# Kernel tuning notes

Hardware: AMD Instinct MI355X
Metric: run time of the kernel (lower is better)

## Reference

```python
import jax, jax.numpy as jnp
import numpy as np

BINS = 32
MAX_DIST = 128
EMB = 1024
DQ = 64
DV = 64
H = 16
B = 8
L = 1024


def _t5_bucket_table():
    # matches: clamp(n,max=m) + (log(clamp(n,min=m)-m+1)*(bins-1-m)/log(max_distance-m+1)).long()
    n = np.arange(MAX_DIST + 1)
    m = BINS // 2
    idx = np.minimum(n, m) + (
        np.log(np.maximum(n, m) - m + 1) * (BINS - 1 - m) / np.log(MAX_DIST - m + 1)
    ).astype(np.int64)
    return jnp.asarray(idx)


def setup_inputs() -> dict:
    key = jax.random.key(0)
    ks = jax.random.split(key, 8)
    s = 0.02
    return {
        "x": jax.random.normal(ks[0], (B, L, EMB), dtype=jnp.float32),
        "qk_w": jax.random.normal(ks[1], (2 * DQ * H, EMB), dtype=jnp.float32) * s,
        "qk_b": jnp.zeros((2 * DQ * H,), dtype=jnp.float32),
        "v_w": jax.random.normal(ks[2], (DV * H, EMB), dtype=jnp.float32) * s,
        "v_b": jnp.zeros((DV * H,), dtype=jnp.float32),
        "out_w": jax.random.normal(ks[3], (EMB, DV * H), dtype=jnp.float32) * s,
        "out_b": jnp.zeros((EMB,), dtype=jnp.float32),
        "bias": jax.random.normal(ks[4], (BINS, H), dtype=jnp.float32) * s,  # causal -> bins rows
    }


def reference(x, qk_w, qk_b, v_w, v_b, out_w, out_b, bias):
    # projections
    qk = (x @ qk_w.T + qk_b).reshape(B, L, H, 2 * DQ).transpose(0, 2, 1, 3)  # [B,H,L,2DQ]
    q, k = qk[..., :DQ], qk[..., DQ:]
    v = (x @ v_w.T + v_b).reshape(B, L, H, DV).transpose(0, 2, 1, 3)  # [B,H,L,DV]

    # T5 relative-position bias (causal): gather per (i-j) distance bucket
    idx_tab = _t5_bucket_table()
    shifts = jnp.arange(L)[:, None] - jnp.arange(L)[None, :]  # [L,L], i - j
    bins_idx = idx_tab[jnp.clip(jnp.abs(shifts), 0, MAX_DIST)]  # [L,L]
    bmat = bias[bins_idx].transpose(2, 0, 1)  # [H,L,L]
    bmat = jnp.where(shifts < 0, -jnp.inf, bmat)  # causal mask (j > i)

    scale = 1.0 / np.sqrt(DQ).astype(np.float32)
    scores = jnp.einsum("bhid,bhjd->bhij", q, k) * scale + bmat  # [B,H,L,L]
    attn = jax.nn.softmax(scores, axis=-1)
    out = jnp.einsum("bhij,bhjd->bhid", attn, v)  # [B,H,L,DV]
    out = out.transpose(0, 2, 1, 3).reshape(B, L, H * DV)
    return out @ out_w.T + out_b
```

## Files before the change

kernel.cpp:

```cpp
#include <hip/hip_runtime.h>
#include <cmath>


typedef _Float16 f16x8 __attribute__((ext_vector_type(8)));
typedef _Float16 f16x4 __attribute__((ext_vector_type(4)));
typedef float    f32x4 __attribute__((ext_vector_type(4)));

#define NEG_INF (-__builtin_inff())
#define LOG2E 1.4426950408889634f

#if __has_builtin(__builtin_amdgcn_exp2f)
#define EXP2(x) __builtin_amdgcn_exp2f(x)
#else
#define EXP2(x) exp2f(x)
#endif

__device__ __forceinline__ void gl_lds16(const void* g, void* l) {
  __builtin_amdgcn_global_load_lds(
      (__attribute__((address_space(1))) void*)g,
      (__attribute__((address_space(3))) void*)l,
      16, 0, 0);
}

__device__ __forceinline__ f32x4 mfma32(f16x8 a, f16x8 b, f32x4 c) {
  return __builtin_amdgcn_mfma_f32_16x16x32_f16(a, b, c, 0, 0, 0);
}
__device__ __forceinline__ f32x4 mfma16(f16x4 a, f16x4 b, f32x4 c) {
  return __builtin_amdgcn_mfma_f32_16x16x16f16(a, b, c, 0, 0, 0);
}

typedef __attribute__((address_space(3))) _Float16* lds_f16p;

#define DSR(d, a, o) \
  asm volatile("ds_read_b128 %0, %1 offset:" o : "=v"(d) : "v"(a))

#define GEMM_VM4 asm volatile("s_waitcnt vmcnt(4)" ::: "memory")
#define GEMM_VM3 asm volatile("s_waitcnt vmcnt(3)" ::: "memory")
#define GEMM_VM0 asm volatile("s_waitcnt vmcnt(0)" ::: "memory")
#define GEMM_BAR __builtin_amdgcn_s_barrier()

#define GEMM_COMPUTE(aB, bB)                             \
  do {                                                   \
    f16x8 af0, af1, af2, af3, bf0, bf1, bf2, bf3;        \
    DSR(af0, aB, "0");                                   \
    DSR(bf0, bB, "0");                                   \
    DSR(af1, aB, "1024");                                \
    DSR(bf1, bB, "1024");                                \
    DSR(af2, aB, "2048");                                \
    DSR(bf2, bB, "2048");                                \
    DSR(af3, aB, "3072");                                \
    DSR(bf3, bB, "3072");                                \
    asm volatile("s_waitcnt lgkmcnt(4)" ::: "memory");   \
    __builtin_amdgcn_sched_barrier(0);                   \
    __builtin_amdgcn_s_setprio(1);                       \
    acc[0][0] = mfma32(af0, bf0, acc[0][0]);             \
    acc[0][1] = mfma32(af0, bf1, acc[0][1]);             \
    acc[1][0] = mfma32(af1, bf0, acc[1][0]);             \
    acc[1][1] = mfma32(af1, bf1, acc[1][1]);             \
    asm volatile("s_waitcnt lgkmcnt(0)" ::: "memory");   \
    __builtin_amdgcn_sched_barrier(0);                   \
    acc[0][2] = mfma32(af0, bf2, acc[0][2]);             \
    acc[0][3] = mfma32(af0, bf3, acc[0][3]);             \
    acc[1][2] = mfma32(af1, bf2, acc[1][2]);             \
    acc[1][3] = mfma32(af1, bf3, acc[1][3]);             \
    acc[2][0] = mfma32(af2, bf0, acc[2][0]);             \
    acc[2][1] = mfma32(af2, bf1, acc[2][1]);             \
    acc[2][2] = mfma32(af2, bf2, acc[2][2]);             \
    acc[2][3] = mfma32(af2, bf3, acc[2][3]);             \
    acc[3][0] = mfma32(af3, bf0, acc[3][0]);             \
    acc[3][1] = mfma32(af3, bf1, acc[3][1]);             \
    acc[3][2] = mfma32(af3, bf2, acc[3][2]);             \
    acc[3][3] = mfma32(af3, bf3, acc[3][3]);             \
    __builtin_amdgcn_s_setprio(0);                       \
  } while (0)

__global__ void cvt4_kernel(const float* __restrict__ x,
                            const float* __restrict__ w1,
                            const float* __restrict__ w2,
                            const float* __restrict__ w3,
                            _Float16* __restrict__ ox, _Float16* __restrict__ o1,
                            _Float16* __restrict__ o2, _Float16* __restrict__ o3) {
  const int bid = blockIdx.x;
  const float* src;
  _Float16* dst;
  int idx;
  if (bid < 8192) {
    src = x; dst = ox; idx = bid * 256 + threadIdx.x;
  } else if (bid < 10240) {
    src = w1; dst = o1; idx = (bid - 8192) * 256 + threadIdx.x;
  } else if (bid < 11264) {
    src = w2; dst = o2; idx = (bid - 10240) * 256 + threadIdx.x;
  } else {
    src = w3; dst = o3; idx = (bid - 11264) * 256 + threadIdx.x;
  }
  float4 v = reinterpret_cast<const float4*>(src)[idx];
  f16x4 o;
  o[0] = (_Float16)v.x; o[1] = (_Float16)v.y;
  o[2] = (_Float16)v.z; o[3] = (_Float16)v.w;
  reinterpret_cast<f16x4*>(dst)[idx] = o;
}

#define GEMM_STAGE256(buf, kk)                                \
  do {                                                        \
    gl_lds16(pA0 + (kk), &lds[(buf)*8192 + wof]);             \
    gl_lds16(pA1 + (kk), &lds[(buf)*8192 + 4096 + wof]);      \
    gl_lds16(pB0 + (kk), &lds[24576 + (buf)*4096 + wof]);     \
  } while (0)

__global__ __launch_bounds__(512, 4) void gemm256_kernel(
    const _Float16* __restrict__ A, const _Float16* __restrict__ Bm,
    const float* __restrict__ bias_q, const float* __restrict__ bias_v,
    _Float16* __restrict__ qkbuf, _Float16* __restrict__ vtbuf) {
  const int K = 1024;
  __shared__ __align__(16) _Float16 lds[36864];
  const int t = threadIdx.x;
  const int w = t >> 6;
  const int lane = t & 63;
  const int lq = lane & 15, lg = lane >> 4;
  const int wr = w >> 1, wc = w & 1;
  const int m0 = blockIdx.y * 256, n0 = blockIdx.x * 128;

  const int stc = ((t & 3) ^ ((t >> 3) & 3)) * 8;
  const _Float16* pA0 = A + (size_t)(m0 + (t >> 2)) * K + stc;
  const _Float16* pA1 = pA0 + (size_t)128 * K;
  const _Float16* pB0 = Bm + (size_t)(n0 + (t >> 2)) * K + stc;
  const int wof = w * 512;

  const int xsw = (lq >> 1) & 3;
  const uint32_t base = (uint32_t)(uintptr_t)(lds_f16p)&lds[0];
  const uint32_t aB0 =
      base + (uint32_t)((wr * 64 + lq) * 64 + ((lg ^ xsw) << 4));
  const uint32_t aB1 = aB0 + 16384;
  const uint32_t aB2 = aB0 + 32768;
  const uint32_t bB0 =
      base + 49152 + (uint32_t)((wc * 64 + lq) * 64 + ((lg ^ xsw) << 4));
  const uint32_t bB1 = bB0 + 8192;
  const uint32_t bB2 = bB0 + 16384;

  f32x4 acc[4][4];
#pragma unroll
  for (int mi = 0; mi < 4; ++mi)
#pragma unroll
    for (int ni = 0; ni < 4; ++ni) acc[mi][ni] = (f32x4){0.f, 0.f, 0.f, 0.f};

  GEMM_STAGE256(0, 0);
  GEMM_STAGE256(1, 32);
  for (int kt = 0; kt < 960; kt += 96) {
    GEMM_VM3;
    GEMM_BAR;
    GEMM_STAGE256(2, kt + 64);
    GEMM_COMPUTE(aB0, bB0);
    GEMM_VM3;
    GEMM_BAR;
    GEMM_STAGE256(0, kt + 96);
    GEMM_COMPUTE(aB1, bB1);
    GEMM_VM3;
    GEMM_BAR;
    GEMM_STAGE256(1, kt + 128);
    GEMM_COMPUTE(aB2, bB2);
  }
  GEMM_VM3;
  GEMM_BAR;
  GEMM_COMPUTE(aB0, bB0);
  GEMM_VM0;
  GEMM_BAR;
  GEMM_COMPUTE(aB1, bB1);

  GEMM_BAR;
  _Float16* T = &lds[0];
  const bool isqk = (n0 < 2048);
  const int bb = m0 >> 10, ii0 = m0 & 1023;
  if (isqk) {
#pragma unroll
    for (int mi = 0; mi < 4; ++mi)
#pragma unroll
      for (int ni = 0; ni < 4; ++ni) {
        const int col = wc * 64 + ni * 16 + lq;
        const float bq = bias_q[n0 + col];
#pragma unroll
        for (int r = 0; r < 4; ++r) {
          const int row = wr * 64 + mi * 16 + lg * 4 + r;
          T[row * 136 + col] = (_Float16)(acc[mi][ni][r] + bq);
        }
      }
    __syncthreads();
    const int hh = n0 >> 7;
    _Float16* gb = qkbuf + ((size_t)((bb * 16 + hh) * 1024 + ii0)) * 128;
    const int row = t >> 1, half = t & 1;
    const int so = row * 136 + half * 64;
    const int go = row * 128 + half * 64;
#pragma unroll
    for (int j = 0; j < 8; ++j)
      *(f16x8*)(gb + go + j * 8) = *(const f16x8*)&T[so + j * 8];
  } else {
    const int nn0 = n0 - 2048;
#pragma unroll
    for (int mi = 0; mi < 4; ++mi)
#pragma unroll
      for (int ni = 0; ni < 4; ++ni) {
        const int col = wc * 64 + ni * 16 + lq;
        const float bv = bias_v[nn0 + col];
        const int row0 = wr * 64 + mi * 16 + lg * 4;
        f16x4 p;
#pragma unroll
        for (int r = 0; r < 4; ++r) p[r] = (_Float16)(acc[mi][ni][r] + bv);
        *(f16x4*)&T[col * 264 + row0] = p;
      }
    __syncthreads();
    const int c = t >> 2, qd = t & 3;
    const int nn = nn0 + c;
    const int hh = nn >> 6, dv = nn & 63;
    _Float16* gb = vtbuf + ((size_t)((bb * 16 + hh) * 64 + dv)) * 1024 +
                   ii0 + qd * 64;
    const int so = c * 264 + qd * 64;
#pragma unroll
    for (int j = 0; j < 8; ++j)
      *(f16x8*)(gb + j * 8) = *(const f16x8*)&T[so + j * 8];
  }
}

#define GEMM_STAGE128(buf, kk)                                     \
  do {                                                             \
    gl_lds16(pA0 + (kk), &lds[(buf)*4096 + wof]);                  \
    gl_lds16(pA1 + (kk), &lds[(buf)*4096 + 2048 + wof]);           \
    gl_lds16(pB0 + (kk), &lds[12288 + (buf)*4096 + wof]);          \
    gl_lds16(pB1 + (kk), &lds[12288 + (buf)*4096 + 2048 + wof]);   \
  } while (0)

__global__ __launch_bounds__(256, 3) void gemm128_kernel(
    const _Float16* __restrict__ A, const _Float16* __restrict__ Bm,
    const float* __restrict__ bias_o, float* __restrict__ outf) {
  const int K = 1024, N = 1024;
  __shared__ __align__(16) _Float16 lds[6 * 4096];
  const int t = threadIdx.x;
  const int w = t >> 6;
  const int lane = t & 63;
  const int lq = lane & 15, lg = lane >> 4;
  const int wr = w >> 1, wc = w & 1;
  const int m0 = blockIdx.y * 128, n0 = blockIdx.x * 128;

  const int stc = ((t & 3) ^ ((t >> 3) & 3)) * 8;
  const _Float16* pA0 = A + (size_t)(m0 + (t >> 2)) * K + stc;
  const _Float16* pA1 = pA0 + (size_t)64 * K;
  const _Float16* pB0 = Bm + (size_t)(n0 + (t >> 2)) * K + stc;
  const _Float16* pB1 = pB0 + (size_t)64 * K;
  const int wof = w * 512;

  const int xsw = (lq >> 1) & 3;
  const uint32_t base = (uint32_t)(uintptr_t)(lds_f16p)&lds[0];
  const uint32_t aB0 =
      base + (uint32_t)((wr * 64 + lq) * 64 + ((lg ^ xsw) << 4));
  const uint32_t aB1 = aB0 + 8192;
  const uint32_t aB2 = aB0 + 16384;
  const uint32_t bB0 =
      base + 24576 + (uint32_t)((wc * 64 + lq) * 64 + ((lg ^ xsw) << 4));
  const uint32_t bB1 = bB0 + 8192;
  const uint32_t bB2 = bB0 + 16384;

  f32x4 acc[4][4];
#pragma unroll
  for (int mi = 0; mi < 4; ++mi)
#pragma unroll
    for (int ni = 0; ni < 4; ++ni) acc[mi][ni] = (f32x4){0.f, 0.f, 0.f, 0.f};

  GEMM_STAGE128(0, 0);
  GEMM_STAGE128(1, 32);
  for (int kt = 0; kt < 960; kt += 96) {
    GEMM_VM4;
    GEMM_BAR;
    GEMM_STAGE128(2, kt + 64);
    GEMM_COMPUTE(aB0, bB0);
    GEMM_VM4;
    GEMM_BAR;
    GEMM_STAGE128(0, kt + 96);
    GEMM_COMPUTE(aB1, bB1);
    GEMM_VM4;
    GEMM_BAR;
    GEMM_STAGE128(1, kt + 128);
    GEMM_COMPUTE(aB2, bB2);
  }
  GEMM_VM4;
  GEMM_BAR;
  GEMM_COMPUTE(aB0, bB0);
  GEMM_VM0;
  GEMM_BAR;
  GEMM_COMPUTE(aB1, bB1);

#pragma unroll
  for (int mi = 0; mi < 4; ++mi)
#pragma unroll
    for (int ni = 0; ni < 4; ++ni)
#pragma unroll
      for (int r = 0; r < 4; ++r) {
        const int mg = m0 + wr * 64 + mi * 16 + lg * 4 + r;
        const int ng = n0 + wc * 64 + ni * 16 + lq;
        outf[(size_t)mg * N + ng] = acc[mi][ni][r] + bias_o[ng];
      }
}

__device__ __forceinline__ void stage_kv(const _Float16* __restrict__ kb,
                                         const _Float16* __restrict__ vtb,
                                         int j0, _Float16* kl, _Float16* vl,
                                         int t) {
  const int r0 = t >> 3, c0 = t & 7;
  const int r1 = r0 + 32;
  const int kc0 = c0 ^ (r0 & 7), kc1 = c0 ^ (r1 & 7);
  gl_lds16(kb + (size_t)(j0 + r0) * 128 + kc0 * 8, kl + t * 8);
  gl_lds16(kb + (size_t)(j0 + r1) * 128 + kc1 * 8, kl + (t + 256) * 8);
  gl_lds16(vtb + (size_t)r0 * 1024 + j0 + kc0 * 8, vl + t * 8);
  gl_lds16(vtb + (size_t)r1 * 1024 + j0 + kc1 * 8, vl + (t + 256) * 8);
}

__device__ __forceinline__ void softmax16(f32x4 (&st)[4], f16x4 (&ph)[4],
                                          int qi, int j0, bool far,
                                          const float* __restrict__ tab,
                                          float t128, int lg4, float& m_run,
                                          float& l_part, f32x4 (&oacc)[4]) {
  float xs[16];
  float lmax = NEG_INF;
  if (far) {
#pragma unroll
    for (int js = 0; js < 4; ++js)
#pragma unroll
      for (int r = 0; r < 4; ++r) {
        const float xv = fmaf(st[js][r], 0.125f * LOG2E, t128);
        xs[js * 4 + r] = xv;
        lmax = fmaxf(lmax, xv);
      }
  } else {
#pragma unroll
    for (int js = 0; js < 4; ++js)
#pragma unroll
      for (int r = 0; r < 4; ++r) {
        const int jj = j0 + js * 16 + lg4 + r;
        const int dd = qi - jj;
        const int idx = dd < 0 ? 0 : (dd > 128 ? 128 : dd);
        const float xv =
            (dd < 0) ? NEG_INF : fmaf(st[js][r], 0.125f * LOG2E, tab[idx]);
        xs[js * 4 + r] = xv;
        lmax = fmaxf(lmax, xv);
      }
  }
  if (__any(lmax > m_run + 8.0f)) {
    float tmax = fmaxf(lmax, __shfl_xor(lmax, 16));
    tmax = fmaxf(tmax, __shfl_xor(tmax, 32));
    const float m_new = fmaxf(m_run, tmax);
    const float sf = EXP2(m_run - m_new);
    m_run = m_new;
    l_part *= sf;
    f32x4 sfv;
#pragma unroll
    for (int r = 0; r < 4; ++r) sfv[r] = __shfl(sf, lg4 + r);
#pragma unroll
    for (int db = 0; db < 4; ++db) oacc[db] *= sfv;
  }
  float ls = 0.f;
#pragma unroll
  for (int js = 0; js < 4; ++js)
#pragma unroll
    for (int r = 0; r < 4; ++r) {
      const float p = EXP2(xs[js * 4 + r] - m_run);
      ls += p;
      ph[js][r] = (_Float16)p;
    }
  l_part += ls;
}

__global__ __launch_bounds__(256, 4) void attn_kernel(
    const _Float16* __restrict__ qk,
    const _Float16* __restrict__ vt,
    const float* __restrict__ bias,
    _Float16* __restrict__ ao) {
  __shared__ __align__(16) _Float16 kls[2][64 * 64];
  __shared__ __align__(16) _Float16 vls[2][64 * 64];
  __shared__ float tab[132];
  const int t = threadIdx.x;
  const int bid = blockIdx.x;
  const int bh = (bid & 7) * 16 + (bid >> 6);
  const int b4 = (bid >> 3) & 7;
  const int h = bh & 15, b = bh >> 4;
  if (t < 129) {
    const int bucket =
        (t <= 16) ? t : 16 + (int)(log((double)(t - 15)) * 15.0 / log(113.0));
    tab[t] = bias[bucket * 16 + h] * LOG2E;
  }

  const int w = t >> 6, lane = t & 63;
  const int lq = lane & 15, lg = lane >> 4;
  const int lg4 = lg * 4, lg8 = lg * 8;
  const int tA = b4, tB = 15 - b4;
  const int q0A = tA * 64 + w * 16, q0B = tB * 64 + w * 16;
  const int qA = q0A + lq, qB = q0B + lq;
  const _Float16* qkb = qk + (size_t)bh * 1024 * 128;
  const _Float16* kb = qkb + 64;
  const _Float16* vtb = vt + (size_t)bh * 64 * 1024;

  const f16x8 qfA0 = *(const f16x8*)&qkb[qA * 128 + lg8];
  const f16x8 qfA1 = *(const f16x8*)&qkb[qA * 128 + 32 + lg8];
  const f16x8 qfB0 = *(const f16x8*)&qkb[qB * 128 + lg8];
  const f16x8 qfB1 = *(const f16x8*)&qkb[qB * 128 + 32 + lg8];

  f32x4 oA[4], oB[4];
#pragma unroll
  for (int db = 0; db < 4; ++db) {
    oA[db] = (f32x4){0.f, 0.f, 0.f, 0.f};
    oB[db] = (f32x4){0.f, 0.f, 0.f, 0.f};
  }
  float mA = NEG_INF, lAp = 0.f, mB = NEG_INF, lBp = 0.f;

  stage_kv(kb, vtb, 0, kls[0], vls[0], t);
  __syncthreads();
  const float t128 = tab[128];
  const int krsw = lq & 7;
  const int vsw = (lq & 7) << 1;
  int cur = 0;

  for (int jt = 0; jt <= tB; ++jt) {
    const int j0 = jt * 64;
    if (jt < tB) stage_kv(kb, vtb, j0 + 64, kls[cur ^ 1], vls[cur ^ 1], t);
    const bool aact = (jt <= tA);
    const _Float16* kbf = kls[cur];
    const _Float16* vbf = vls[cur];

    f32x4 stA[4], stB[4];
#pragma unroll
    for (int js = 0; js < 4; ++js) {
      const int rowb = (js * 16 + lq) * 64;
      const f16x8 kf0 = *(const f16x8*)&kbf[rowb + ((lg ^ krsw) << 3)];
      const f16x8 kf1 = *(const f16x8*)&kbf[rowb + (((lg + 4) ^ krsw) << 3)];
      if (aact) {
        stA[js] = mfma32(kf0, qfA0, (f32x4){0.f, 0.f, 0.f, 0.f});
        stA[js] = mfma32(kf1, qfA1, stA[js]);
      }
      stB[js] = mfma32(kf0, qfB0, (f32x4){0.f, 0.f, 0.f, 0.f});
      stB[js] = mfma32(kf1, qfB1, stB[js]);
    }

    f16x4 phA[4], phB[4];
    if (aact)
      softmax16(stA, phA, qA, j0, q0A - j0 >= 192, tab, t128, lg4, mA, lAp,
                oA);
    softmax16(stB, phB, qB, j0, q0B - j0 >= 192, tab, t128, lg4, mB, lBp, oB);

#pragma unroll
    for (int js = 0; js < 4; ++js)
#pragma unroll
      for (int db = 0; db < 4; ++db) {
        const f16x4 vf = *(const f16x4*)&vbf[(db * 16 + lq) * 64 +
                                             ((((js << 2) + lg) ^ vsw) << 2)];
        if (aact) oA[db] = mfma16(phA[js], vf, oA[db]);
        oB[db] = mfma16(phB[js], vf, oB[db]);
      }

    __syncthreads();
    cur ^= 1;
  }

  _Float16* aob = ao + ((size_t)b * 1024) * 1024 + h * 64;
  {
    float lt = lAp + __shfl_xor(lAp, 16);
    lt += __shfl_xor(lt, 32);
    f32x4 linv;
#pragma unroll
    for (int r = 0; r < 4; ++r) linv[r] = 1.0f / __shfl(lt, lg4 + r);
#pragma unroll
    for (int db = 0; db < 4; ++db)
#pragma unroll
      for (int r = 0; r < 4; ++r)
        aob[(size_t)(q0A + lg4 + r) * 1024 + db * 16 + lq] =
            (_Float16)(oA[db][r] * linv[r]);
  }
  {
    float lt = lBp + __shfl_xor(lBp, 16);
    lt += __shfl_xor(lt, 32);
    f32x4 linv;
#pragma unroll
    for (int r = 0; r < 4; ++r) linv[r] = 1.0f / __shfl(lt, lg4 + r);
#pragma unroll
    for (int db = 0; db < 4; ++db)
#pragma unroll
      for (int r = 0; r < 4; ++r)
        aob[(size_t)(q0B + lg4 + r) * 1024 + db * 16 + lq] =
            (_Float16)(oB[db][r] * linv[r]);
  }
}

extern "C" void kernel_launch(void* const* d_in, const int* in_sizes, int n_in,
                              void* d_out, int out_size, void* d_ws,
                              size_t ws_size, hipStream_t stream) {
  const float* x = (const float*)d_in[0];
  const float* qk_w = (const float*)d_in[1];
  const float* qk_b = (const float*)d_in[2];
  const float* v_w = (const float*)d_in[3];
  const float* v_b = (const float*)d_in[4];
  const float* out_w = (const float*)d_in[5];
  const float* out_b = (const float*)d_in[6];
  const float* bias = (const float*)d_in[7];
  float* out = (float*)d_out;

  _Float16* xb = (_Float16*)d_ws;
  _Float16* wb = xb + (size_t)8388608;
  _Float16* owb = wb + (size_t)3145728;
  _Float16* qkbuf = owb + (size_t)1048576;
  _Float16* vtbuf = qkbuf + (size_t)16777216;
  _Float16* ao = vtbuf + (size_t)8388608;

  cvt4_kernel<<<12288, 256, 0, stream>>>(x, qk_w, v_w, out_w, xb, wb,
                                         wb + 2097152, owb);

  gemm256_kernel<<<dim3(24, 32), 512, 0, stream>>>(xb, wb, qk_b, v_b, qkbuf,
                                                   vtbuf);

  attn_kernel<<<1024, 256, 0, stream>>>(qkbuf, vtbuf, bias, ao);

  gemm128_kernel<<<dim3(8, 64), 256, 0, stream>>>(ao, owb, out_b, out);
}
```

Measured before the change: 162.7 us.

## Use 4-wave 256x128 QKV GEMM tile with larger per-wave 64x128 subtiles

The QKV projection GEMM keeps its 256x128 block tile but moves from 8 waves (512 threads), each computing 64x64, to 4 waves (256 threads), each computing 64x128 with a 4x8 MFMA accumulator grid. Each wave now reuses its A fragments across twice as many B fragments, which cuts LDS read traffic per MFMA, and staging issues six global-to-LDS loads per thread instead of three. The cost is much higher register pressure (128 accumulator VGPRs plus 12 fragment registers), occupancy held to 2 blocks per CU, and fewer waves available to hide latency. The epilogue writes are reworked to match the new thread count.

```diff
diff --git a/kernel.cpp b/kernel.cpp
--- a/kernel.cpp
+++ b/kernel.cpp
@@ -34,10 +34,192 @@
 #define DSR(d, a, o) \
   asm volatile("ds_read_b128 %0, %1 offset:" o : "=v"(d) : "v"(a))
 
+#define GEMM_VM6 asm volatile("s_waitcnt vmcnt(6)" ::: "memory")
 #define GEMM_VM4 asm volatile("s_waitcnt vmcnt(4)" ::: "memory")
-#define GEMM_VM3 asm volatile("s_waitcnt vmcnt(3)" ::: "memory")
 #define GEMM_VM0 asm volatile("s_waitcnt vmcnt(0)" ::: "memory")
 #define GEMM_BAR __builtin_amdgcn_s_barrier()
+
+__global__ void cvt4_kernel(const float* __restrict__ x,
+                            const float* __restrict__ w1,
+                            const float* __restrict__ w2,
+                            const float* __restrict__ w3,
+                            _Float16* __restrict__ ox, _Float16* __restrict__ o1,
+                            _Float16* __restrict__ o2, _Float16* __restrict__ o3) {
+  const int bid = blockIdx.x;
+  const float* src;
+  _Float16* dst;
+  int idx;
+  if (bid < 8192) {
+    src = x; dst = ox; idx = bid * 256 + threadIdx.x;
+  } else if (bid < 10240) {
+    src = w1; dst = o1; idx = (bid - 8192) * 256 + threadIdx.x;
+  } else if (bid < 11264) {
+    src = w2; dst = o2; idx = (bid - 10240) * 256 + threadIdx.x;
+  } else {
+    src = w3; dst = o3; idx = (bid - 11264) * 256 + threadIdx.x;
+  }
+  float4 v = reinterpret_cast<const float4*>(src)[idx];
+  f16x4 o;
+  o[0] = (_Float16)v.x; o[1] = (_Float16)v.y;
+  o[2] = (_Float16)v.z; o[3] = (_Float16)v.w;
+  reinterpret_cast<f16x4*>(dst)[idx] = o;
+}
+
+#define GEMM_STAGEW(buf, kk)                                        \
+  do {                                                              \
+    gl_lds16(pA0 + (kk), &lds[(buf)*8192 + wof]);                   \
+    gl_lds16(pA1 + (kk), &lds[(buf)*8192 + 2048 + wof]);            \
+    gl_lds16(pA2 + (kk), &lds[(buf)*8192 + 4096 + wof]);            \
+    gl_lds16(pA3 + (kk), &lds[(buf)*8192 + 6144 + wof]);            \
+    gl_lds16(pB0 + (kk), &lds[24576 + (buf)*4096 + wof]);           \
+    gl_lds16(pB1 + (kk), &lds[24576 + (buf)*4096 + 2048 + wof]);    \
+  } while (0)
+
+#define GEMM_COMPUTEW(aB, bB)                                  \
+  do {                                                         \
+    f16x8 af[4], bf[8];                                        \
+    DSR(af[0], aB, "0");                                       \
+    DSR(af[1], aB, "1024");                                    \
+    DSR(af[2], aB, "2048");                                    \
+    DSR(af[3], aB, "3072");                                    \
+    DSR(bf[0], bB, "0");                                       \
+    DSR(bf[1], bB, "1024");                                    \
+    DSR(bf[2], bB, "2048");                                    \
+    DSR(bf[3], bB, "3072");                                    \
+    DSR(bf[4], bB, "4096");                                    \
+    DSR(bf[5], bB, "5120");                                    \
+    DSR(bf[6], bB, "6144");                                    \
+    DSR(bf[7], bB, "7168");                                    \
+    asm volatile("s_waitcnt lgkmcnt(6)" ::: "memory");         \
+    __builtin_amdgcn_sched_barrier(0);                         \
+    __builtin_amdgcn_s_setprio(1);                             \
+    _Pragma("unroll") for (int mi = 0; mi < 4; ++mi)           \
+      _Pragma("unroll") for (int ni = 0; ni < 2; ++ni)         \
+        acc[mi][ni] = mfma32(af[mi], bf[ni], acc[mi][ni]);     \
+    asm volatile("s_waitcnt lgkmcnt(0)" ::: "memory");         \
+    __builtin_amdgcn_sched_barrier(0);                         \
+    _Pragma("unroll") for (int mi = 0; mi < 4; ++mi)           \
+      _Pragma("unroll") for (int ni = 2; ni < 8; ++ni)         \
+        acc[mi][ni] = mfma32(af[mi], bf[ni], acc[mi][ni]);     \
+    __builtin_amdgcn_s_setprio(0);                             \
+  } while (0)
+
+__global__ __launch_bounds__(256, 2) void gemmw_kernel(
+    const _Float16* __restrict__ A, const _Float16* __restrict__ Bm,
+    const float* __restrict__ bias_q, const float* __restrict__ bias_v,
+    _Float16* __restrict__ qkbuf, _Float16* __restrict__ vtbuf) {
+  const int K = 1024;
+  __shared__ __align__(16) _Float16 lds[36864];
+  const int t = threadIdx.x;
+  const int w = t >> 6;
+  const int lane = t & 63;
+  const int lq = lane & 15, lg = lane >> 4;
+  const int m0 = blockIdx.y * 256, n0 = blockIdx.x * 128;
+
+  const int stc = ((t & 3) ^ ((t >> 3) & 3)) * 8;
+  const _Float16* pA0 = A + (size_t)(m0 + (t >> 2)) * K + stc;
+  const _Float16* pA1 = pA0 + (size_t)64 * K;
+  const _Float16* pA2 = pA0 + (size_t)128 * K;
+  const _Float16* pA3 = pA0 + (size_t)192 * K;
+  const _Float16* pB0 = Bm + (size_t)(n0 + (t >> 2)) * K + stc;
+  const _Float16* pB1 = pB0 + (size_t)64 * K;
+  const int wof = w * 512;
+
+  const int xsw = (lq >> 1) & 3;
+  const uint32_t base = (uint32_t)(uintptr_t)(lds_f16p)&lds[0];
+  const uint32_t aB0 =
+      base + (uint32_t)((w * 64 + lq) * 64 + ((lg ^ xsw) << 4));
+  const uint32_t aB1 = aB0 + 16384;
+  const uint32_t aB2 = aB0 + 32768;
+  const uint32_t bB0 =
+      base + 49152 + (uint32_t)(lq * 64 + ((lg ^ xsw) << 4));
+  const uint32_t bB1 = bB0 + 8192;
+  const uint32_t bB2 = bB0 + 16384;
+
+  f32x4 acc[4][8];
+#pragma unroll
+  for (int mi = 0; mi < 4; ++mi)
+#pragma unroll
+    for (int ni = 0; ni < 8; ++ni) acc[mi][ni] = (f32x4){0.f, 0.f, 0.f, 0.f};
+
+  GEMM_STAGEW(0, 0);
+  GEMM_STAGEW(1, 32);
+  for (int kt = 0; kt < 960; kt += 96) {
+    GEMM_VM6;
+    GEMM_BAR;
+    GEMM_STAGEW(2, kt + 64);
+    GEMM_COMPUTEW(aB0, bB0);
+    GEMM_VM6;
+    GEMM_BAR;
+    GEMM_STAGEW(0, kt + 96);
+    GEMM_COMPUTEW(aB1, bB1);
+    GEMM_VM6;
+    GEMM_BAR;
+    GEMM_STAGEW(1, kt + 128);
+    GEMM_COMPUTEW(aB2, bB2);
+  }
+  GEMM_VM6;
+  GEMM_BAR;
+  GEMM_COMPUTEW(aB0, bB0);
+  GEMM_VM0;
+  GEMM_BAR;
+  GEMM_COMPUTEW(aB1, bB1);
+
+  GEMM_BAR;
+  _Float16* T = &lds[0];
+  const bool isqk = (n0 < 2048);
+  const int bb = m0 >> 10, ii0 = m0 & 1023;
+  if (isqk) {
+#pragma unroll
+    for (int mi = 0; mi < 4; ++mi)
+#pragma unroll
+      for (int ni = 0; ni < 8; ++ni) {
+        const int col = ni * 16 + lq;
+        const float bq = bias_q[n0 + col];
+#pragma unroll
+        for (int r = 0; r < 4; ++r) {
+          const int row = w * 64 + mi * 16 + lg * 4 + r;
+          T[row * 136 + col] = (_Float16)(acc[mi][ni][r] + bq);
+        }
+      }
+    __syncthreads();
+    const int hh = n0 >> 7;
+    _Float16* gb = qkbuf + ((size_t)((bb * 16 + hh) * 1024 + ii0)) * 128;
+#pragma unroll
+    for (int h2 = 0; h2 < 2; ++h2) {
+      const int row = h2 * 128 + (t >> 1);
+      const int so = row * 136 + (t & 1) * 64;
+      const int go = row * 128 + (t & 1) * 64;
+#pragma unroll
+      for (int j = 0; j < 8; ++j)
+        *(f16x8*)(gb + go + j * 8) = *(const f16x8*)&T[so + j * 8];
+    }
+  } else {
+    const int nn0 = n0 - 2048;
+#pragma unroll
+    for (int mi = 0; mi < 4; ++mi)
+#pragma unroll
+      for (int ni = 0; ni < 8; ++ni) {
+        const int col = ni * 16 + lq;
+        const float bv = bias_v[nn0 + col];
+        const int row0 = w * 64 + mi * 16 + lg * 4;
+        f16x4 p;
+#pragma unroll
+        for (int r = 0; r < 4; ++r) p[r] = (_Float16)(acc[mi][ni][r] + bv);
+        *(f16x4*)&T[col * 264 + row0] = p;
+      }
+    __syncthreads();
+    const int c = t >> 1, half = t & 1;
+    const int nn = nn0 + c;
+    const int hh = nn >> 6, dv = nn & 63;
+    _Float16* gb = vtbuf + ((size_t)((bb * 16 + hh) * 64 + dv)) * 1024 +
+                   ii0 + half * 128;
+    const int so = c * 264 + half * 128;
+#pragma unroll
+    for (int j = 0; j < 16; ++j)
+      *(f16x8*)(gb + j * 8) = *(const f16x8*)&T[so + j * 8];
+  }
+}
 
 #define GEMM_COMPUTE(aB, bB)                             \
   do {                                                   \
@@ -74,151 +256,6 @@
     __builtin_amdgcn_s_setprio(0);                       \
   } while (0)
 
-__global__ void cvt4_kernel(const float* __restrict__ x,
-                            const float* __restrict__ w1,
-                            const float* __restrict__ w2,
-                            const float* __restrict__ w3,
-                            _Float16* __restrict__ ox, _Float16* __restrict__ o1,
-                            _Float16* __restrict__ o2, _Float16* __restrict__ o3) {
-  const int bid = blockIdx.x;
-  const float* src;
-  _Float16* dst;
-  int idx;
-  if (bid < 8192) {
-    src = x; dst = ox; idx = bid * 256 + threadIdx.x;
-  } else if (bid < 10240) {
-    src = w1; dst = o1; idx = (bid - 8192) * 256 + threadIdx.x;
-  } else if (bid < 11264) {
-    src = w2; dst = o2; idx = (bid - 10240) * 256 + threadIdx.x;
-  } else {
-    src = w3; dst = o3; idx = (bid - 11264) * 256 + threadIdx.x;
-  }
-  float4 v = reinterpret_cast<const float4*>(src)[idx];
-  f16x4 o;
-  o[0] = (_Float16)v.x; o[1] = (_Float16)v.y;
-  o[2] = (_Float16)v.z; o[3] = (_Float16)v.w;
-  reinterpret_cast<f16x4*>(dst)[idx] = o;
-}
-
-#define GEMM_STAGE256(buf, kk)                                \
-  do {                                                        \
-    gl_lds16(pA0 + (kk), &lds[(buf)*8192 + wof]);             \
-    gl_lds16(pA1 + (kk), &lds[(buf)*8192 + 4096 + wof]);      \
-    gl_lds16(pB0 + (kk), &lds[24576 + (buf)*4096 + wof]);     \
-  } while (0)
-
-__global__ __launch_bounds__(512, 4) void gemm256_kernel(
-    const _Float16* __restrict__ A, const _Float16* __restrict__ Bm,
-    const float* __restrict__ bias_q, const float* __restrict__ bias_v,
-    _Float16* __restrict__ qkbuf, _Float16* __restrict__ vtbuf) {
-  const int K = 1024;
-  __shared__ __align__(16) _Float16 lds[36864];
-  const int t = threadIdx.x;
-  const int w = t >> 6;
-  const int lane = t & 63;
-  const int lq = lane & 15, lg = lane >> 4;
-  const int wr = w >> 1, wc = w & 1;
-  const int m0 = blockIdx.y * 256, n0 = blockIdx.x * 128;
-
-  const int stc = ((t & 3) ^ ((t >> 3) & 3)) * 8;
-  const _Float16* pA0 = A + (size_t)(m0 + (t >> 2)) * K + stc;
-  const _Float16* pA1 = pA0 + (size_t)128 * K;
-  const _Float16* pB0 = Bm + (size_t)(n0 + (t >> 2)) * K + stc;
-  const int wof = w * 512;
-
-  const int xsw = (lq >> 1) & 3;
-  const uint32_t base = (uint32_t)(uintptr_t)(lds_f16p)&lds[0];
-  const uint32_t aB0 =
-      base + (uint32_t)((wr * 64 + lq) * 64 + ((lg ^ xsw) << 4));
-  const uint32_t aB1 = aB0 + 16384;
-  const uint32_t aB2 = aB0 + 32768;
-  const uint32_t bB0 =
-      base + 49152 + (uint32_t)((wc * 64 + lq) * 64 + ((lg ^ xsw) << 4));
-  const uint32_t bB1 = bB0 + 8192;
-  const uint32_t bB2 = bB0 + 16384;
-
-  f32x4 acc[4][4];
-#pragma unroll
-  for (int mi = 0; mi < 4; ++mi)
-#pragma unroll
-    for (int ni = 0; ni < 4; ++ni) acc[mi][ni] = (f32x4){0.f, 0.f, 0.f, 0.f};
-
-  GEMM_STAGE256(0, 0);
-  GEMM_STAGE256(1, 32);
-  for (int kt = 0; kt < 960; kt += 96) {
-    GEMM_VM3;
-    GEMM_BAR;
-    GEMM_STAGE256(2, kt + 64);
-    GEMM_COMPUTE(aB0, bB0);
-    GEMM_VM3;
-    GEMM_BAR;
-    GEMM_STAGE256(0, kt + 96);
-    GEMM_COMPUTE(aB1, bB1);
-    GEMM_VM3;
-    GEMM_BAR;
-    GEMM_STAGE256(1, kt + 128);
-    GEMM_COMPUTE(aB2, bB2);
-  }
-  GEMM_VM3;
-  GEMM_BAR;
-  GEMM_COMPUTE(aB0, bB0);
-  GEMM_VM0;
-  GEMM_BAR;
-  GEMM_COMPUTE(aB1, bB1);
-
-  GEMM_BAR;
-  _Float16* T = &lds[0];
-  const bool isqk = (n0 < 2048);
-  const int bb = m0 >> 10, ii0 = m0 & 1023;
-  if (isqk) {
-#pragma unroll
-    for (int mi = 0; mi < 4; ++mi)
-#pragma unroll
-      for (int ni = 0; ni < 4; ++ni) {
-        const int col = wc * 64 + ni * 16 + lq;
-        const float bq = bias_q[n0 + col];
-#pragma unroll
-        for (int r = 0; r < 4; ++r) {
-          const int row = wr * 64 + mi * 16 + lg * 4 + r;
-          T[row * 136 + col] = (_Float16)(acc[mi][ni][r] + bq);
-        }
-      }
-    __syncthreads();
-    const int hh = n0 >> 7;
-    _Float16* gb = qkbuf + ((size_t)((bb * 16 + hh) * 1024 + ii0)) * 128;
-    const int row = t >> 1, half = t & 1;
-    const int so = row * 136 + half * 64;
-    const int go = row * 128 + half * 64;
-#pragma unroll
-    for (int j = 0; j < 8; ++j)
-      *(f16x8*)(gb + go + j * 8) = *(const f16x8*)&T[so + j * 8];
-  } else {
-    const int nn0 = n0 - 2048;
-#pragma unroll
-    for (int mi = 0; mi < 4; ++mi)
-#pragma unroll
-      for (int ni = 0; ni < 4; ++ni) {
-        const int col = wc * 64 + ni * 16 + lq;
-        const float bv = bias_v[nn0 + col];
-        const int row0 = wr * 64 + mi * 16 + lg * 4;
-        f16x4 p;
-#pragma unroll
-        for (int r = 0; r < 4; ++r) p[r] = (_Float16)(acc[mi][ni][r] + bv);
-        *(f16x4*)&T[col * 264 + row0] = p;
-      }
-    __syncthreads();
-    const int c = t >> 2, qd = t & 3;
-    const int nn = nn0 + c;
-    const int hh = nn >> 6, dv = nn & 63;
-    _Float16* gb = vtbuf + ((size_t)((bb * 16 + hh) * 64 + dv)) * 1024 +
-                   ii0 + qd * 64;
-    const int so = c * 264 + qd * 64;
-#pragma unroll
-    for (int j = 0; j < 8; ++j)
-      *(f16x8*)(gb + j * 8) = *(const f16x8*)&T[so + j * 8];
-  }
-}
-
 #define GEMM_STAGE128(buf, kk)                                     \
   do {                                                             \
     gl_lds16(pA0 + (kk), &lds[(buf)*4096 + wof]);                  \
@@ -508,8 +545,8 @@
   cvt4_kernel<<<12288, 256, 0, stream>>>(x, qk_w, v_w, out_w, xb, wb,
                                          wb + 2097152, owb);
 
-  gemm256_kernel<<<dim3(24, 32), 512, 0, stream>>>(xb, wb, qk_b, v_b, qkbuf,
-                                                   vtbuf);
+  gemmw_kernel<<<dim3(24, 32), 256, 0, stream>>>(xb, wb, qk_b, v_b, qkbuf,
+                                                 vtbuf);
 
   attn_kernel<<<1024, 256, 0, stream>>>(qkbuf, vtbuf, bias, ao);
 
```

Measured after the change: 160.5 us. About the same (-1.4%).
